# Optimization experiments

Measured on AMD Instinct MI355X. Metric: run time of the kernel, lower is better.

## Reference

```python
import jax, jax.numpy as jnp
import numpy as np

NUM_TREE = 64
DEPTH = 7
INPUT_FEATURE = 1024
BATCH = 32768
LEAF = 2 ** (DEPTH - 1)  # 64


def setup_inputs() -> dict:
    key = jax.random.key(0)
    k1, k2 = jax.random.split(key, 2)
    x = jax.random.normal(k1, (BATCH, INPUT_FEATURE), dtype=jnp.float32)
    # each tree picks leaf_num-1 distinct feature columns (one-hot matmul == gather)
    rng = np.random.default_rng(0)
    idx = np.stack([rng.choice(INPUT_FEATURE, LEAF - 1, replace=False)
                    for _ in range(NUM_TREE)]).astype(np.int32)
    feature_idx = jnp.asarray(idx)  # [T, L-1]
    # pi.get_mean(): leaf means, np.random.rand -> uniform [0,1)
    pi = jax.random.uniform(k2, (NUM_TREE, LEAF), dtype=jnp.float32)
    return {"x": x, "feature_idx": feature_idx, "pi": pi}


def reference(x, feature_idx, pi):
    T, Lm1 = feature_idx.shape
    leaf = Lm1 + 1
    depth = int(np.log2(leaf)) + 1  # static
    B = x.shape[0]
    # torch.mm(x, one_hot_feature) == column gather; sigmoid routing decisions
    d = jax.nn.sigmoid(x[:, feature_idx])  # [B, T, L-1]
    # recursive cumulative-product leaf probabilities over tree layers (BFS order)
    mu = jnp.ones((B, T, 1), dtype=x.dtype)
    begin = 0
    for layer in range(depth - 1):
        n = 2 ** layer
        dl = d[:, :, begin:begin + n]  # [B, T, n]
        # child order per node: (left=sigmoid, right=1-sigmoid), interleaved
        mu = jnp.stack([mu * dl, mu * (1.0 - dl)], axis=-1).reshape(B, T, 2 * n)
        begin += n
    # mu: [B, T, L] leaf probabilities per tree
    prob = jnp.einsum('btl,tl->bt', mu, pi)        # [B, T]
    probs = jnp.transpose(mu, (0, 2, 1))           # [B, L, T] (matches torch layout)
    return prob, probs
```

## Files before the change

kernel.cpp:

```cpp
#include <hip/hip_runtime.h>

#define NTREE  64
#define NFEAT  1024
#define NLEAF  64
#define NBATCH 32768
#define WAVES  4
#define THREADS 256

__global__ __launch_bounds__(THREADS)
void forest_kernel(const float* __restrict__ x,
                   const int*   __restrict__ fidx,
                   const float* __restrict__ pi,
                   float* __restrict__ prob,
                   float* __restrict__ probs)
{
    __shared__ float srow[WAVES][NFEAT];
    __shared__ int   idxl[NTREE * 63];
    __shared__ float pil[NTREE * 65];

    const int tid  = threadIdx.x;
    const int wid  = tid >> 6;
    const int lane = tid & 63;

    for (int i = tid; i < NTREE * 63; i += THREADS) idxl[i] = fidx[i];
    for (int i = tid; i < NTREE * NLEAF; i += THREADS)
        pil[(i >> 6) * 65 + (i & 63)] = pi[i];
    __syncthreads();

    const int wavestride = gridDim.x * WAVES;
    for (int b = blockIdx.x * WAVES + wid; b < NBATCH; b += wavestride) {
        const float4* xr4 = reinterpret_cast<const float4*>(x + (size_t)b * NFEAT);
        float4* sr4 = reinterpret_cast<float4*>(&srow[wid][0]);
        #pragma unroll
        for (int i = 0; i < NFEAT / (64 * 4); ++i) {
            float4 v = xr4[lane + i * 64];
            float4 s;
            s.x = 1.0f / (1.0f + __expf(-v.x));
            s.y = 1.0f / (1.0f + __expf(-v.y));
            s.z = 1.0f / (1.0f + __expf(-v.z));
            s.w = 1.0f / (1.0f + __expf(-v.w));
            sr4[lane + i * 64] = s;
        }
        __syncthreads();

        const int t = lane;
        const float* sw = &srow[wid][0];
        const int ib = t * 63;

        float mu[32];
        mu[0] = 1.0f;
        #pragma unroll
        for (int k = 0; k < 5; ++k) {
            const int n = 1 << k;
            #pragma unroll
            for (int i = n - 1; i >= 0; --i) {
                float dv = sw[idxl[ib + (n - 1) + i]];
                float m  = mu[i];
                float a  = m * dv;
                mu[2 * i]     = a;
                mu[2 * i + 1] = m - a;
            }
        }

        float acc = 0.0f;
        float* pb = probs + (size_t)b * (NLEAF * NTREE) + t;
        const int ip = t * 65;
        #pragma unroll
        for (int i = 0; i < 32; ++i) {
            float dv = sw[idxl[ib + 31 + i]];
            float m  = mu[i];
            float a  = m * dv;
            float c  = m - a;
            pb[(2 * i) * NTREE]     = a;
            pb[(2 * i + 1) * NTREE] = c;
            acc = fmaf(a, pil[ip + 2 * i], acc);
            acc = fmaf(c, pil[ip + 2 * i + 1], acc);
        }
        prob[b * NTREE + t] = acc;
        __syncthreads();
    }
}

extern "C" void kernel_launch(void* const* d_in, const int* in_sizes, int n_in,
                              void* d_out, int out_size, void* d_ws, size_t ws_size,
                              hipStream_t stream) {
    const float* x    = (const float*)d_in[0];
    const int*   fidx = (const int*)d_in[1];
    const float* pi   = (const float*)d_in[2];
    float* prob  = (float*)d_out;
    float* probs = (float*)d_out + (size_t)NBATCH * NTREE;

    dim3 grid(2048), block(THREADS);
    hipLaunchKernelGGL(forest_kernel, grid, block, 0, stream,
                       x, fidx, pi, prob, probs);
}
```

Before: 137.7 us.

## Prefetch next row into registers, drop block barriers, transpose LDS tables

Each wave now loads its next batch row into registers while it computes on the current one, so global loads overlap with compute. Block-wide __syncthreads are replaced by per-wave lgkmcnt waits. The index and pi tables are transposed into lane-contiguous LDS layouts, and the indices are stored as pre-shifted 16-bit byte offsets, to cut bank conflicts and address arithmetic. The division in the sigmoid becomes a hardware reciprocal. These changes add register pressure from the prefetch, slightly reduce sigmoid precision, and rely on per-wave LDS ordering being correct without block barriers.

```diff
diff --git a/kernel.cpp b/kernel.cpp
--- a/kernel.cpp
+++ b/kernel.cpp
@@ -6,46 +6,70 @@
 #define NBATCH 32768
 #define WAVES  4
 #define THREADS 256
+#define GRID   2048
+#define WSTRIDE (GRID * WAVES)
 
-__global__ __launch_bounds__(THREADS)
+__device__ __forceinline__ float sig1(float v) {
+    return __builtin_amdgcn_rcpf(1.0f + __expf(-v));
+}
+__device__ __forceinline__ float4 sig4(float4 v) {
+    return make_float4(sig1(v.x), sig1(v.y), sig1(v.z), sig1(v.w));
+}
+
+__global__ __launch_bounds__(THREADS, 4)
 void forest_kernel(const float* __restrict__ x,
                    const int*   __restrict__ fidx,
                    const float* __restrict__ pi,
                    float* __restrict__ prob,
                    float* __restrict__ probs)
 {
-    __shared__ float srow[WAVES][NFEAT];
-    __shared__ int   idxl[NTREE * 63];
-    __shared__ float pil[NTREE * 65];
+    __shared__ float          srow[WAVES][NFEAT];
+    __shared__ float          pil[NLEAF * NTREE];
+    __shared__ unsigned short idxl[63 * 64];
 
     const int tid  = threadIdx.x;
     const int wid  = tid >> 6;
     const int lane = tid & 63;
 
-    for (int i = tid; i < NTREE * 63; i += THREADS) idxl[i] = fidx[i];
-    for (int i = tid; i < NTREE * NLEAF; i += THREADS)
-        pil[(i >> 6) * 65 + (i & 63)] = pi[i];
+    for (int i = tid; i < 63 * 64; i += THREADS) {
+        int t = i / 63, c = i - t * 63;
+        idxl[c * 64 + t] = (unsigned short)(fidx[i] << 2);
+    }
+    for (int i = tid; i < NTREE * NLEAF; i += THREADS) {
+        int t = i >> 6, l = i & 63;
+        pil[l * 64 + t] = pi[i];
+    }
     __syncthreads();
 
-    const int wavestride = gridDim.x * WAVES;
-    for (int b = blockIdx.x * WAVES + wid; b < NBATCH; b += wavestride) {
-        const float4* xr4 = reinterpret_cast<const float4*>(x + (size_t)b * NFEAT);
-        float4* sr4 = reinterpret_cast<float4*>(&srow[wid][0]);
-        #pragma unroll
-        for (int i = 0; i < NFEAT / (64 * 4); ++i) {
-            float4 v = xr4[lane + i * 64];
-            float4 s;
-            s.x = 1.0f / (1.0f + __expf(-v.x));
-            s.y = 1.0f / (1.0f + __expf(-v.y));
-            s.z = 1.0f / (1.0f + __expf(-v.z));
-            s.w = 1.0f / (1.0f + __expf(-v.w));
-            sr4[lane + i * 64] = s;
+    const int t = lane;
+    float* sw = &srow[wid][0];
+
+    int b = blockIdx.x * WAVES + wid;
+    const float4* xr4 = reinterpret_cast<const float4*>(x + (size_t)b * NFEAT);
+    float4 c0 = xr4[lane];
+    float4 c1 = xr4[lane + 64];
+    float4 c2 = xr4[lane + 128];
+    float4 c3 = xr4[lane + 192];
+
+    #pragma unroll 1
+    for (int it = 0; it < NBATCH / WSTRIDE; ++it, b += WSTRIDE) {
+        float4* sr4 = reinterpret_cast<float4*>(sw);
+        sr4[lane      ] = sig4(c0);
+        sr4[lane +  64] = sig4(c1);
+        sr4[lane + 128] = sig4(c2);
+        sr4[lane + 192] = sig4(c3);
+
+        int bn = b + WSTRIDE;
+        if (bn < NBATCH) {
+            const float4* nx = reinterpret_cast<const float4*>(x + (size_t)bn * NFEAT);
+            c0 = nx[lane];
+            c1 = nx[lane + 64];
+            c2 = nx[lane + 128];
+            c3 = nx[lane + 192];
         }
-        __syncthreads();
 
-        const int t = lane;
-        const float* sw = &srow[wid][0];
-        const int ib = t * 63;
+        asm volatile("s_waitcnt lgkmcnt(0)" ::: "memory");
+        __builtin_amdgcn_sched_barrier(0);
 
         float mu[32];
         mu[0] = 1.0f;
@@ -54,7 +78,7 @@
             const int n = 1 << k;
             #pragma unroll
             for (int i = n - 1; i >= 0; --i) {
-                float dv = sw[idxl[ib + (n - 1) + i]];
+                float dv = *(const float*)((const char*)sw + idxl[(n - 1 + i) * 64 + t]);
                 float m  = mu[i];
                 float a  = m * dv;
                 mu[2 * i]     = a;
@@ -64,20 +88,20 @@
 
         float acc = 0.0f;
         float* pb = probs + (size_t)b * (NLEAF * NTREE) + t;
-        const int ip = t * 65;
         #pragma unroll
         for (int i = 0; i < 32; ++i) {
-            float dv = sw[idxl[ib + 31 + i]];
+            float dv = *(const float*)((const char*)sw + idxl[(31 + i) * 64 + t]);
             float m  = mu[i];
             float a  = m * dv;
             float c  = m - a;
             pb[(2 * i) * NTREE]     = a;
             pb[(2 * i + 1) * NTREE] = c;
-            acc = fmaf(a, pil[ip + 2 * i], acc);
-            acc = fmaf(c, pil[ip + 2 * i + 1], acc);
+            acc = fmaf(a, pil[(2 * i) * 64 + t], acc);
+            acc = fmaf(c, pil[(2 * i + 1) * 64 + t], acc);
         }
         prob[b * NTREE + t] = acc;
-        __syncthreads();
+
+        asm volatile("s_waitcnt lgkmcnt(0)" ::: "memory");
     }
 }
 
@@ -90,7 +114,7 @@
     float* prob  = (float*)d_out;
     float* probs = (float*)d_out + (size_t)NBATCH * NTREE;
 
-    dim3 grid(2048), block(THREADS);
+    dim3 grid(GRID), block(THREADS);
     hipLaunchKernelGGL(forest_kernel, grid, block, 0, stream,
                        x, fidx, pi, prob, probs);
 }
```

Result: slower. 141.1 us (+2.5%).
